# Kernel tuning notes

Measured on AMD Instinct MI355X. Metric: run time of the kernel, lower is better.

Reference implementation:

```python
import jax, jax.numpy as jnp
import numpy as np

N = 1024            # samples per branch
C = 64              # num_classes == embedding dim
MARGIN = 15.0       # self.margin and args.margin
LAM = 0.5           # args.lam
PROTOTYPE_POSITION = 1.0  # args.prototype_position
EPS_JS = 1e-8

def _cdist(a, b):
    # torch.cdist(p=2) via the gram trick; clamp for sqrt stability
    d2 = jnp.sum(a * a, axis=1)[:, None] + jnp.sum(b * b, axis=1)[None, :] - 2.0 * (a @ b.T)
    return jnp.sqrt(jnp.maximum(d2, 1e-12))

def _js_matrix(A, B):
    # pairwise Jensen-Shannon divergence: A [NA,C], B [NB,C] -> [NA,NB]
    A = A + EPS_JS
    B = B + EPS_JS
    logM = jnp.log((A[:, None, :] + B[None, :, :]) * 0.5)   # [NA,NB,C]
    kl_am = jnp.sum(A[:, None, :] * (jnp.log(A)[:, None, :] - logM), axis=-1)
    kl_bm = jnp.sum(B[None, :, :] * (jnp.log(B)[None, :, :] - logM), axis=-1)
    return 0.5 * kl_am + 0.5 * kl_bm

def _positive_branch(x, l_soft, x_prob):
    onehot = jnp.eye(C, dtype=x.dtype)
    # JS coefficient is computed via numpy in torch -> constant (no grad)
    js = jax.lax.stop_gradient(1.0 - _js_matrix(x_prob, onehot))       # [N, C]
    diff = x[:, None, :] - onehot * PROTOTYPE_POSITION                 # [N, C, C]
    pos_dist = jnp.sqrt(jnp.maximum(jnp.sum(diff * diff, axis=2), 1e-12))
    return jnp.sum(pos_dist * l_soft * js, axis=1)                     # [N]

def _ood_branch(x, branch_centers):
    d = _cdist(x, branch_centers)                                      # [N, C]
    ood_dist = jnp.maximum(MARGIN - d, 0.0)  # one_hot_labels are all ones
    coffi = jax.lax.stop_gradient(jnp.min(1.0 - ood_dist / MARGIN, axis=1))
    variance = jnp.sum((ood_dist / MARGIN) ** 2, axis=1)
    return variance * coffi                                            # [N]

def setup_inputs():
    key = jax.random.key(0)
    ks = jax.random.split(key, 6)
    x1 = jax.random.normal(ks[0], (N, C), jnp.float32)
    x2 = jax.random.normal(ks[1], (N, C), jnp.float32)
    x_prob1 = jax.nn.softmax(jax.random.normal(ks[2], (N, C), jnp.float32), axis=-1)
    x_prob2 = jax.nn.softmax(jax.random.normal(ks[3], (N, C), jnp.float32), axis=-1)
    l1 = jax.random.uniform(ks[4], (N, C), jnp.float32)
    l1 = l1 / jnp.sum(l1, axis=1, keepdims=True)
    l2 = jax.random.uniform(ks[5], (N, C), jnp.float32)
    l2 = l2 / jnp.sum(l2, axis=1, keepdims=True)
    # args.prototypes: class prototypes at scaled one-hot positions
    branch_centers = jnp.eye(C, dtype=jnp.float32) * PROTOTYPE_POSITION
    return {"x1": x1, "x2": x2, "x_prob1": x_prob1, "x_prob2": x_prob2,
            "l1": l1, "l2": l2, "branch_centers": branch_centers}

def reference(x1, x2, x_prob1, x_prob2, l1, l2, branch_centers):
    # positive loss
    posi = 0.5 * (jnp.sum(_positive_branch(x1, l1, x_prob1))
                  + jnp.sum(_positive_branch(x2, l2, x_prob2)))
    # negative loss
    neg_coffi = 1.0 - l1 @ l2.T                                        # [N, N]
    js = jax.lax.stop_gradient(_js_matrix(x_prob1, x_prob2))           # [N, N]
    ed = _cdist(x1, x2) + 1e-10
    pairs = jnp.maximum(MARGIN - ed, 0.0) * neg_coffi * js
    counts = jnp.sum(pairs > 0, axis=1)
    counts = jnp.where(counts == 0, 1, counts).astype(pairs.dtype)
    nega = jnp.sum(jnp.sum(pairs, axis=1) / counts)
    # ood loss
    ood = 0.5 * (jnp.sum(_ood_branch(x1, branch_centers))
                 + jnp.sum(_ood_branch(x2, branch_centers)))
    loss = posi + nega + LAM * ood
    return (loss, posi, nega)
```

## Files before the change

kernel.cpp:

```cpp
#include <hip/hip_runtime.h>

#define NN 1024
#define CC 64
#define MARGINF 15.0f
#define EPSJ 1e-8f
#define LN2F 0.69314718056f

#define C1_OFF   0
#define C2_OFF   (NN)
#define Q1_OFF   (2 * NN)
#define Q2_OFF   (3 * NN)
#define PP_OFF   (4 * NN)
#define OP_OFF   (4 * NN + 512)
#define NS_OFF   (4 * NN + 1024)
#define NC_OFF   (4 * NN + 1024 + 32 * NN)

__global__ __launch_bounds__(256) void fused_row_kernel(
    const float* __restrict__ x1, const float* __restrict__ x2,
    const float* __restrict__ p1, const float* __restrict__ p2,
    const float* __restrict__ l1, const float* __restrict__ l2,
    float* __restrict__ ws)
{
    const float S_B_CONST = -1.1595029e-5f;
    const float RSB_CONST = 1.00000064f;
    __shared__ float sposi[4], sood[4];

    int wave = (blockIdx.x * 256 + threadIdx.x) >> 6;
    int lane = threadIdx.x & 63;
    int wib  = threadIdx.x >> 6;
    int i = wave & (NN - 1);
    bool second = wave >= NN;
    const float* x = second ? x2 : x1;
    const float* p = second ? p2 : p1;
    const float* l = second ? l2 : l1;

    float P  = p[i * CC + lane];
    float xv = x[i * CC + lane];
    float lv = l[i * CC + lane];
    float A     = P + EPSJ;
    float AlogA = A * __logf(A);
    float t     = A + EPSJ;
    float tlogt = t * __logf(t);
    float xs    = xv * xv;

    float sA = AlogA, rsA = A, V = tlogt, q = xs;
    #pragma unroll
    for (int m = 32; m >= 1; m >>= 1) {
        sA  += __shfl_xor(sA,  m, 64);
        rsA += __shfl_xor(rsA, m, 64);
        V   += __shfl_xor(V,   m, 64);
        q   += __shfl_xor(q,   m, 64);
    }

    if (lane == 0) {
        ws[C1_OFF + (second ? NN : 0) + i] = sA + LN2F * rsA;
        ws[Q1_OFF + (second ? NN : 0) + i] = q;
    }

    float w = A + (1.0f + EPSJ);
    float sumslogs = V - tlogt + w * __logf(w);
    float js_div = 0.5f * (sA + S_B_CONST - sumslogs + LN2F * (rsA + RSB_CONST));
    float js = 1.0f - js_div;
    float pd = sqrtf(fmaxf(q - 2.0f * xv + 1.0f, 1e-12f));
    float posv = pd * lv * js;

    float od  = fmaxf(MARGINF - pd, 0.0f);
    float r   = od * (1.0f / MARGINF);
    float var = r * r;
    float cof = 1.0f - r;
    #pragma unroll
    for (int m = 32; m >= 1; m >>= 1) {
        posv += __shfl_xor(posv, m, 64);
        var  += __shfl_xor(var,  m, 64);
        cof   = fminf(cof, __shfl_xor(cof, m, 64));
    }
    if (lane == 0) {
        sposi[wib] = posv;
        sood[wib]  = var * cof;
    }
    __syncthreads();
    if (threadIdx.x == 0) {
        ws[PP_OFF + blockIdx.x] = sposi[0] + sposi[1] + sposi[2] + sposi[3];
        ws[OP_OFF + blockIdx.x] = sood[0] + sood[1] + sood[2] + sood[3];
    }
}

__global__ __launch_bounds__(256) void neg_kernel(
    const float* __restrict__ x1, const float* __restrict__ x2,
    const float* __restrict__ p1, const float* __restrict__ p2,
    const float* __restrict__ l1, const float* __restrict__ l2,
    float* __restrict__ ws)
{
    __shared__ float sx1[32][36], sp1[32][36], sl1[32][36];
    __shared__ float sx2[32][36], sp2[32][36], sl2[32][36];

    int t  = threadIdx.x;
    int bx = blockIdx.x, by = blockIdx.y;
    int i0 = by * 32, j0 = bx * 32;
    int tx = t & 15, ty = t >> 4;

    float K2[2][2] = {{0.f,0.f},{0.f,0.f}};
    float G[2][2]  = {{0.f,0.f},{0.f,0.f}};
    float H[2][2]  = {{0.f,0.f},{0.f,0.f}};

    for (int ph = 0; ph < 2; ++ph) {
        if (ph) __syncthreads();
        {
            int row = t >> 3;
            int col = (t & 7) * 4;
            int ga  = (i0 + row) * CC + ph * 32 + col;
            int gb  = (j0 + row) * CC + ph * 32 + col;
            float4 v;
            v = *(const float4*)&x1[ga];                         *(float4*)&sx1[row][col] = v;
            v = *(const float4*)&p1[ga];
            v.x += EPSJ; v.y += EPSJ; v.z += EPSJ; v.w += EPSJ;  *(float4*)&sp1[row][col] = v;
            v = *(const float4*)&l1[ga];                         *(float4*)&sl1[row][col] = v;
            v = *(const float4*)&x2[gb];                         *(float4*)&sx2[row][col] = v;
            v = *(const float4*)&p2[gb];
            v.x += EPSJ; v.y += EPSJ; v.z += EPSJ; v.w += EPSJ;  *(float4*)&sp2[row][col] = v;
            v = *(const float4*)&l2[gb];                         *(float4*)&sl2[row][col] = v;
        }
        __syncthreads();

        for (int cg = 0; cg < 8; ++cg) {
            int c = cg * 4;
            float4 ap[2], ax[2], alv[2], bp[2], bx4[2], blv[2];
            #pragma unroll
            for (int r = 0; r < 2; r++) {
                int ir = ty + 16 * r;
                int jr = tx + 16 * r;
                ap[r]  = *(float4*)&sp1[ir][c];
                ax[r]  = *(float4*)&sx1[ir][c];
                alv[r] = *(float4*)&sl1[ir][c];
                bp[r]  = *(float4*)&sp2[jr][c];
                bx4[r] = *(float4*)&sx2[jr][c];
                blv[r] = *(float4*)&sl2[jr][c];
            }
            #pragma unroll
            for (int r = 0; r < 2; r++) {
                #pragma unroll
                for (int s = 0; s < 2; s++) {
                    float sv;
                    sv = ap[r].x + bp[s].x; K2[r][s] = fmaf(sv, __log2f(sv), K2[r][s]);
                    G[r][s] = fmaf(ax[r].x, bx4[s].x, G[r][s]);
                    H[r][s] = fmaf(alv[r].x, blv[s].x, H[r][s]);
                    sv = ap[r].y + bp[s].y; K2[r][s] = fmaf(sv, __log2f(sv), K2[r][s]);
                    G[r][s] = fmaf(ax[r].y, bx4[s].y, G[r][s]);
                    H[r][s] = fmaf(alv[r].y, blv[s].y, H[r][s]);
                    sv = ap[r].z + bp[s].z; K2[r][s] = fmaf(sv, __log2f(sv), K2[r][s]);
                    G[r][s] = fmaf(ax[r].z, bx4[s].z, G[r][s]);
                    H[r][s] = fmaf(alv[r].z, blv[s].z, H[r][s]);
                    sv = ap[r].w + bp[s].w; K2[r][s] = fmaf(sv, __log2f(sv), K2[r][s]);
                    G[r][s] = fmaf(ax[r].w, bx4[s].w, G[r][s]);
                    H[r][s] = fmaf(alv[r].w, blv[s].w, H[r][s]);
                }
            }
        }
    }

    const float* c1 = ws + C1_OFF;
    const float* c2 = ws + C2_OFF;
    const float* q1 = ws + Q1_OFF;
    const float* q2 = ws + Q2_OFF;
    float* negS = ws + NS_OFF;
    float* negC = ws + NC_OFF;

    #pragma unroll
    for (int r = 0; r < 2; r++) {
        int gi = i0 + ty + 16 * r;
        float q1v = q1[gi], c1v = c1[gi];
        float psum = 0.0f, pcnt = 0.0f;
        #pragma unroll
        for (int s = 0; s < 2; s++) {
            int gj = j0 + tx + 16 * s;
            float ed = sqrtf(fmaxf(q1v + q2[gj] - 2.0f * G[r][s], 1e-12f)) + 1e-10f;
            float js = 0.5f * (c1v + c2[gj] - LN2F * K2[r][s]);
            float pair = fmaxf(MARGINF - ed, 0.0f) * (1.0f - H[r][s]) * js;
            psum += pair;
            pcnt += (pair > 0.0f) ? 1.0f : 0.0f;
        }
        #pragma unroll
        for (int m = 1; m <= 8; m <<= 1) {
            psum += __shfl_xor(psum, m, 64);
            pcnt += __shfl_xor(pcnt, m, 64);
        }
        if (tx == 0) {
            negS[gi * 32 + bx] = psum;
            negC[gi * 32 + bx] = pcnt;
        }
    }
}

__global__ __launch_bounds__(1024) void final_kernel(
    const float* __restrict__ ws, float* __restrict__ out)
{
    __shared__ float redv[16], redp[16], redo[16];
    int t = threadIdx.x;
    const float* rs = ws + NS_OFF + t * 32;
    const float* rc = ws + NC_OFF + t * 32;
    float s = 0.0f, c = 0.0f;
    #pragma unroll
    for (int k = 0; k < 8; k++) {
        float4 a = *(const float4*)&rs[k * 4];
        float4 b = *(const float4*)&rc[k * 4];
        s += (a.x + a.y) + (a.z + a.w);
        c += (b.x + b.y) + (b.z + b.w);
    }
    float v = s / fmaxf(c, 1.0f);
    float pp = (t < 512) ? ws[PP_OFF + t] : 0.0f;
    float oo = (t < 512) ? ws[OP_OFF + t] : 0.0f;
    #pragma unroll
    for (int m = 32; m >= 1; m >>= 1) {
        v  += __shfl_xor(v,  m, 64);
        pp += __shfl_xor(pp, m, 64);
        oo += __shfl_xor(oo, m, 64);
    }
    if ((t & 63) == 0) { redv[t >> 6] = v; redp[t >> 6] = pp; redo[t >> 6] = oo; }
    __syncthreads();
    if (t < 16) {
        float rv = redv[t], rp = redp[t], ro = redo[t];
        #pragma unroll
        for (int m = 8; m >= 1; m >>= 1) {
            rv += __shfl_xor(rv, m, 16);
            rp += __shfl_xor(rp, m, 16);
            ro += __shfl_xor(ro, m, 16);
        }
        if (t == 0) {
            float nega = rv;
            float posi = 0.5f * rp;
            float ood  = 0.5f * ro;
            out[0] = posi + nega + 0.5f * ood;
            out[1] = posi;
            out[2] = nega;
        }
    }
}

extern "C" void kernel_launch(void* const* d_in, const int* in_sizes, int n_in,
                              void* d_out, int out_size, void* d_ws, size_t ws_size,
                              hipStream_t stream) {
    const float* x1 = (const float*)d_in[0];
    const float* x2 = (const float*)d_in[1];
    const float* p1 = (const float*)d_in[2];
    const float* p2 = (const float*)d_in[3];
    const float* l1 = (const float*)d_in[4];
    const float* l2 = (const float*)d_in[5];
    float* ws  = (float*)d_ws;
    float* out = (float*)d_out;

    hipLaunchKernelGGL(fused_row_kernel, dim3(512), dim3(256), 0, stream,
                       x1, x2, p1, p2, l1, l2, ws);
    hipLaunchKernelGGL(neg_kernel, dim3(32, 32), dim3(256), 0, stream,
                       x1, x2, p1, p2, l1, l2, ws);
    hipLaunchKernelGGL(final_kernel, dim3(1), dim3(1024), 0, stream, ws, out);
}
```

Baseline: 94.66 us.

## Use bf16 MFMA for pairwise dot products and enlarge neg tiles to 64x64

The neg kernel now converts x, p and l tiles to bf16 in shared memory and computes the x1·x2 and l1·l2 Gram terms with 16x16x32 bf16 MFMA instructions instead of scalar FMAs. Tiles grow to 64x64 with 512 threads, and the JS log term is still computed in scalar code from bf16-rounded probabilities. This removes most of the FMA work and halves shared-memory footprint per element. The cost is reduced precision: bf16 rounding of x, l and the probabilities feeding the log terms could push the loss past tolerance.

```diff
diff --git a/kernel.cpp b/kernel.cpp
--- a/kernel.cpp
+++ b/kernel.cpp
@@ -14,6 +14,17 @@
 #define OP_OFF   (4 * NN + 512)
 #define NS_OFF   (4 * NN + 1024)
 #define NC_OFF   (4 * NN + 1024 + 32 * NN)
+
+typedef __attribute__((ext_vector_type(8))) short bf16x8;
+typedef __attribute__((ext_vector_type(4))) float f32x4;
+
+__device__ __forceinline__ unsigned short f2bf(float f) {
+    unsigned int u = __float_as_uint(f);
+    return (unsigned short)((u + 0x7FFFu + ((u >> 16) & 1u)) >> 16);
+}
+__device__ __forceinline__ float bf2f(short s) {
+    return __uint_as_float(((unsigned int)(unsigned short)s) << 16);
+}
 
 __global__ __launch_bounds__(256) void fused_row_kernel(
     const float* __restrict__ x1, const float* __restrict__ x2,
@@ -51,7 +62,6 @@
         V   += __shfl_xor(V,   m, 64);
         q   += __shfl_xor(q,   m, 64);
     }
-
     if (lane == 0) {
         ws[C1_OFF + (second ? NN : 0) + i] = sA + LN2F * rsA;
         ws[Q1_OFF + (second ? NN : 0) + i] = q;
@@ -74,10 +84,7 @@
         var  += __shfl_xor(var,  m, 64);
         cof   = fminf(cof, __shfl_xor(cof, m, 64));
     }
-    if (lane == 0) {
-        sposi[wib] = posv;
-        sood[wib]  = var * cof;
-    }
+    if (lane == 0) { sposi[wib] = posv; sood[wib] = var * cof; }
     __syncthreads();
     if (threadIdx.x == 0) {
         ws[PP_OFF + blockIdx.x] = sposi[0] + sposi[1] + sposi[2] + sposi[3];
@@ -85,75 +92,96 @@
     }
 }
 
-__global__ __launch_bounds__(256) void neg_kernel(
+__global__ __launch_bounds__(512) void neg_kernel(
     const float* __restrict__ x1, const float* __restrict__ x2,
     const float* __restrict__ p1, const float* __restrict__ p2,
     const float* __restrict__ l1, const float* __restrict__ l2,
     float* __restrict__ ws)
 {
-    __shared__ float sx1[32][36], sp1[32][36], sl1[32][36];
-    __shared__ float sx2[32][36], sp2[32][36], sl2[32][36];
-
-    int t  = threadIdx.x;
-    int bx = blockIdx.x, by = blockIdx.y;
-    int i0 = by * 32, j0 = bx * 32;
-    int tx = t & 15, ty = t >> 4;
-
-    float K2[2][2] = {{0.f,0.f},{0.f,0.f}};
-    float G[2][2]  = {{0.f,0.f},{0.f,0.f}};
-    float H[2][2]  = {{0.f,0.f},{0.f,0.f}};
-
-    for (int ph = 0; ph < 2; ++ph) {
-        if (ph) __syncthreads();
-        {
-            int row = t >> 3;
-            int col = (t & 7) * 4;
-            int ga  = (i0 + row) * CC + ph * 32 + col;
-            int gb  = (j0 + row) * CC + ph * 32 + col;
-            float4 v;
-            v = *(const float4*)&x1[ga];                         *(float4*)&sx1[row][col] = v;
-            v = *(const float4*)&p1[ga];
-            v.x += EPSJ; v.y += EPSJ; v.z += EPSJ; v.w += EPSJ;  *(float4*)&sp1[row][col] = v;
-            v = *(const float4*)&l1[ga];                         *(float4*)&sl1[row][col] = v;
-            v = *(const float4*)&x2[gb];                         *(float4*)&sx2[row][col] = v;
-            v = *(const float4*)&p2[gb];
-            v.x += EPSJ; v.y += EPSJ; v.z += EPSJ; v.w += EPSJ;  *(float4*)&sp2[row][col] = v;
-            v = *(const float4*)&l2[gb];                         *(float4*)&sl2[row][col] = v;
-        }
-        __syncthreads();
-
-        for (int cg = 0; cg < 8; ++cg) {
-            int c = cg * 4;
-            float4 ap[2], ax[2], alv[2], bp[2], bx4[2], blv[2];
+    __shared__ unsigned short b1x[64][72], b1p[64][72], b1l[64][72];
+    __shared__ unsigned short b2x[64][72], b2p[64][72], b2l[64][72];
+
+    int t   = threadIdx.x;
+    int bx  = blockIdx.x, by = blockIdx.y;
+    int i0  = by * 64, j0 = bx * 64;
+
+    #pragma unroll
+    for (int k = 0; k < 2; k++) {
+        int f   = t + k * 512;
+        int row = f >> 4;
+        int col = (f & 15) * 4;
+        int ga  = (i0 + row) * CC + col;
+        int gb  = (j0 + row) * CC + col;
+        float4 v; union { unsigned short s[4]; uint2 u; } pk;
+        v = *(const float4*)&x1[ga];
+        pk.s[0]=f2bf(v.x); pk.s[1]=f2bf(v.y); pk.s[2]=f2bf(v.z); pk.s[3]=f2bf(v.w);
+        *(uint2*)&b1x[row][col] = pk.u;
+        v = *(const float4*)&p1[ga];
+        pk.s[0]=f2bf(v.x+EPSJ); pk.s[1]=f2bf(v.y+EPSJ); pk.s[2]=f2bf(v.z+EPSJ); pk.s[3]=f2bf(v.w+EPSJ);
+        *(uint2*)&b1p[row][col] = pk.u;
+        v = *(const float4*)&l1[ga];
+        pk.s[0]=f2bf(v.x); pk.s[1]=f2bf(v.y); pk.s[2]=f2bf(v.z); pk.s[3]=f2bf(v.w);
+        *(uint2*)&b1l[row][col] = pk.u;
+        v = *(const float4*)&x2[gb];
+        pk.s[0]=f2bf(v.x); pk.s[1]=f2bf(v.y); pk.s[2]=f2bf(v.z); pk.s[3]=f2bf(v.w);
+        *(uint2*)&b2x[row][col] = pk.u;
+        v = *(const float4*)&p2[gb];
+        pk.s[0]=f2bf(v.x+EPSJ); pk.s[1]=f2bf(v.y+EPSJ); pk.s[2]=f2bf(v.z+EPSJ); pk.s[3]=f2bf(v.w+EPSJ);
+        *(uint2*)&b2p[row][col] = pk.u;
+        v = *(const float4*)&l2[gb];
+        pk.s[0]=f2bf(v.x); pk.s[1]=f2bf(v.y); pk.s[2]=f2bf(v.z); pk.s[3]=f2bf(v.w);
+        *(uint2*)&b2l[row][col] = pk.u;
+    }
+    __syncthreads();
+
+    int wv  = t >> 6;
+    int ln64 = t & 63;
+    int q   = ln64 >> 4;
+    int ln  = ln64 & 15;
+    int ib  = (wv & 3) * 16;
+    int jh  = (wv >> 2);
+    int jb  = jh * 32;
+
+    f32x4 Gacc[2] = {{0,0,0,0},{0,0,0,0}};
+    f32x4 Hacc[2] = {{0,0,0,0},{0,0,0,0}};
+    {
+        bf16x8 ax0 = *(const bf16x8*)&b1x[ib + ln][q * 8];
+        bf16x8 ax1 = *(const bf16x8*)&b1x[ib + ln][32 + q * 8];
+        bf16x8 al0 = *(const bf16x8*)&b1l[ib + ln][q * 8];
+        bf16x8 al1 = *(const bf16x8*)&b1l[ib + ln][32 + q * 8];
+        #pragma unroll
+        for (int tt = 0; tt < 2; tt++) {
+            int jr = jb + tt * 16 + ln;
+            bf16x8 bx0 = *(const bf16x8*)&b2x[jr][q * 8];
+            bf16x8 bx1 = *(const bf16x8*)&b2x[jr][32 + q * 8];
+            Gacc[tt] = __builtin_amdgcn_mfma_f32_16x16x32_bf16(ax0, bx0, Gacc[tt], 0, 0, 0);
+            Gacc[tt] = __builtin_amdgcn_mfma_f32_16x16x32_bf16(ax1, bx1, Gacc[tt], 0, 0, 0);
+            bf16x8 bl0 = *(const bf16x8*)&b2l[jr][q * 8];
+            bf16x8 bl1 = *(const bf16x8*)&b2l[jr][32 + q * 8];
+            Hacc[tt] = __builtin_amdgcn_mfma_f32_16x16x32_bf16(al0, bl0, Hacc[tt], 0, 0, 0);
+            Hacc[tt] = __builtin_amdgcn_mfma_f32_16x16x32_bf16(al1, bl1, Hacc[tt], 0, 0, 0);
+        }
+    }
+
+    float K2[2][4] = {{0,0,0,0},{0,0,0,0}};
+    #pragma unroll
+    for (int g = 0; g < 8; g++) {
+        bf16x8 apx[4], bpx[2];
+        #pragma unroll
+        for (int v = 0; v < 4; v++)
+            apx[v] = *(const bf16x8*)&b1p[ib + q * 4 + v][g * 8];
+        #pragma unroll
+        for (int tt = 0; tt < 2; tt++)
+            bpx[tt] = *(const bf16x8*)&b2p[jb + tt * 16 + ln][g * 8];
+        #pragma unroll
+        for (int e = 0; e < 8; e++) {
+            float bv0 = bf2f(bpx[0][e]);
+            float bv1 = bf2f(bpx[1][e]);
             #pragma unroll
-            for (int r = 0; r < 2; r++) {
-                int ir = ty + 16 * r;
-                int jr = tx + 16 * r;
-                ap[r]  = *(float4*)&sp1[ir][c];
-                ax[r]  = *(float4*)&sx1[ir][c];
-                alv[r] = *(float4*)&sl1[ir][c];
-                bp[r]  = *(float4*)&sp2[jr][c];
-                bx4[r] = *(float4*)&sx2[jr][c];
-                blv[r] = *(float4*)&sl2[jr][c];
-            }
-            #pragma unroll
-            for (int r = 0; r < 2; r++) {
-                #pragma unroll
-                for (int s = 0; s < 2; s++) {
-                    float sv;
-                    sv = ap[r].x + bp[s].x; K2[r][s] = fmaf(sv, __log2f(sv), K2[r][s]);
-                    G[r][s] = fmaf(ax[r].x, bx4[s].x, G[r][s]);
-                    H[r][s] = fmaf(alv[r].x, blv[s].x, H[r][s]);
-                    sv = ap[r].y + bp[s].y; K2[r][s] = fmaf(sv, __log2f(sv), K2[r][s]);
-                    G[r][s] = fmaf(ax[r].y, bx4[s].y, G[r][s]);
-                    H[r][s] = fmaf(alv[r].y, blv[s].y, H[r][s]);
-                    sv = ap[r].z + bp[s].z; K2[r][s] = fmaf(sv, __log2f(sv), K2[r][s]);
-                    G[r][s] = fmaf(ax[r].z, bx4[s].z, G[r][s]);
-                    H[r][s] = fmaf(alv[r].z, blv[s].z, H[r][s]);
-                    sv = ap[r].w + bp[s].w; K2[r][s] = fmaf(sv, __log2f(sv), K2[r][s]);
-                    G[r][s] = fmaf(ax[r].w, bx4[s].w, G[r][s]);
-                    H[r][s] = fmaf(alv[r].w, blv[s].w, H[r][s]);
-                }
+            for (int v = 0; v < 4; v++) {
+                float av = bf2f(apx[v][e]);
+                float s0 = av + bv0; K2[0][v] = fmaf(s0, __log2f(s0), K2[0][v]);
+                float s1 = av + bv1; K2[1][v] = fmaf(s1, __log2f(s1), K2[1][v]);
             }
         }
     }
@@ -166,16 +194,18 @@
     float* negC = ws + NC_OFF;
 
     #pragma unroll
-    for (int r = 0; r < 2; r++) {
-        int gi = i0 + ty + 16 * r;
+    for (int v = 0; v < 4; v++) {
+        int gi = i0 + ib + q * 4 + v;
         float q1v = q1[gi], c1v = c1[gi];
         float psum = 0.0f, pcnt = 0.0f;
         #pragma unroll
-        for (int s = 0; s < 2; s++) {
-            int gj = j0 + tx + 16 * s;
-            float ed = sqrtf(fmaxf(q1v + q2[gj] - 2.0f * G[r][s], 1e-12f)) + 1e-10f;
-            float js = 0.5f * (c1v + c2[gj] - LN2F * K2[r][s]);
-            float pair = fmaxf(MARGINF - ed, 0.0f) * (1.0f - H[r][s]) * js;
+        for (int tt = 0; tt < 2; tt++) {
+            int gj = j0 + jb + tt * 16 + ln;
+            float Gv = Gacc[tt][v];
+            float Hv = Hacc[tt][v];
+            float ed = sqrtf(fmaxf(q1v + q2[gj] - 2.0f * Gv, 1e-12f)) + 1e-10f;
+            float js = 0.5f * (c1v + c2[gj] - LN2F * K2[tt][v]);
+            float pair = fmaxf(MARGINF - ed, 0.0f) * (1.0f - Hv) * js;
             psum += pair;
             pcnt += (pair > 0.0f) ? 1.0f : 0.0f;
         }
@@ -184,9 +214,9 @@
             psum += __shfl_xor(psum, m, 64);
             pcnt += __shfl_xor(pcnt, m, 64);
         }
-        if (tx == 0) {
-            negS[gi * 32 + bx] = psum;
-            negC[gi * 32 + bx] = pcnt;
+        if (ln == 0) {
+            negS[gi * 32 + bx * 2 + jh] = psum;
+            negC[gi * 32 + bx * 2 + jh] = pcnt;
         }
     }
 }
@@ -250,7 +280,7 @@
 
     hipLaunchKernelGGL(fused_row_kernel, dim3(512), dim3(256), 0, stream,
                        x1, x2, p1, p2, l1, l2, ws);
-    hipLaunchKernelGGL(neg_kernel, dim3(32, 32), dim3(256), 0, stream,
+    hipLaunchKernelGGL(neg_kernel, dim3(16, 16), dim3(512), 0, stream,
                        x1, x2, p1, p2, l1, l2, ws);
     hipLaunchKernelGGL(final_kernel, dim3(1), dim3(1024), 0, stream, ws, out);
 }
```

Result: faster. 91.85 us (-3.0%).
